# Optimization experiments

Measured on AMD Instinct MI355X. Metric: run time of the kernel, lower is better.

## Reference

```python
import jax, jax.numpy as jnp
import numpy as np

DIM = 1024
LATENT = 512
HEADS = 16
HEAD_DIM = DIM // HEADS


def setup_inputs() -> dict:
    key = jax.random.key(0)
    ks = jax.random.split(key, 9)
    s = 0.02
    return {
        "x": jax.random.normal(ks[0], (2, 2048, DIM), dtype=jnp.float32),
        "Wq": jax.random.normal(ks[1], (DIM, DIM), dtype=jnp.float32) * s,
        "Wkv": jax.random.normal(ks[2], (DIM, 2 * DIM), dtype=jnp.float32) * s,
        "Wk1": jax.random.normal(ks[3], (DIM, LATENT), dtype=jnp.float32) * s,
        "Wk2": jax.random.normal(ks[4], (LATENT, DIM), dtype=jnp.float32) * s,
        "Wv1": jax.random.normal(ks[5], (DIM, LATENT), dtype=jnp.float32) * s,
        "Wv2": jax.random.normal(ks[6], (LATENT, DIM), dtype=jnp.float32) * s,
        "Wo": jax.random.normal(ks[7], (DIM, DIM), dtype=jnp.float32) * s,
        "bo": jax.random.normal(ks[8], (DIM,), dtype=jnp.float32) * s,
    }


def reference(x, Wq, Wkv, Wk1, Wk2, Wv1, Wv2, Wo, bo):
    b, n, dim = x.shape
    scale = HEAD_DIM ** -0.5
    q = x @ Wq                               # [b, n, dim]
    kv = x @ Wkv                             # [b, n, 2*dim]
    k, v = kv[..., :dim], kv[..., dim:]
    # latent bottleneck MLPs (Linear -> ReLU -> Linear, no bias)
    k = jax.nn.relu(k @ Wk1) @ Wk2           # [b, n, dim]
    v = jax.nn.relu(v @ Wv1) @ Wv2           # [b, n, dim]
    # split heads: [b, n, h*d] -> [b, h, n, d]
    def split_heads(t):
        return t.reshape(b, n, HEADS, HEAD_DIM).transpose(0, 2, 1, 3)
    q = split_heads(q) * scale
    k = split_heads(k)
    v = split_heads(v)
    scores = jnp.einsum('bhid,bhjd->bhij', q, k)   # [b, h, n, n]
    attn = jax.nn.softmax(scores, axis=-1)
    out = jnp.einsum('bhij,bhjd->bhid', attn, v)   # [b, h, n, d]
    out = out.transpose(0, 2, 1, 3).reshape(b, n, dim)
    return out @ Wo + bo
```

## Files before the change

### kernel.cpp

```cpp
#include <hip/hip_runtime.h>
#include <stdint.h>


typedef __attribute__((ext_vector_type(8))) __bf16 bf16x8;
typedef __attribute__((ext_vector_type(4))) float f32x4;

__device__ inline unsigned short f2bfu(float f) {
    __bf16 b = (__bf16)f;
    return __builtin_bit_cast(unsigned short, b);
}

__device__ inline float exp2_fast(float f) {
    return __builtin_amdgcn_exp2f(f);
}

__device__ inline void load_lds16(const void* g, void* l) {
    __builtin_amdgcn_global_load_lds(
        (const __attribute__((address_space(1))) uint32_t*)g,
        (__attribute__((address_space(3))) uint32_t*)l, 16, 0, 0);
}

__device__ inline f32x4 mfma_bf16(bf16x8 a, bf16x8 b, f32x4 c) {
    return __builtin_amdgcn_mfma_f32_16x16x32_bf16(a, b, c, 0, 0, 0);
}

__global__ __launch_bounds__(256) void prep_kernel(
    const float* __restrict__ x, unsigned short* __restrict__ xb,
    const float* __restrict__ Wq,  const float* __restrict__ Wo,
    const float* __restrict__ Wkv,
    const float* __restrict__ Wk1, const float* __restrict__ Wv1,
    const float* __restrict__ Wk2, const float* __restrict__ Wv2,
    unsigned short* __restrict__ WqkvT, unsigned short* __restrict__ WoT,
    unsigned short* __restrict__ Wk1T,  unsigned short* __restrict__ Wv1T,
    unsigned short* __restrict__ Wk2T,  unsigned short* __restrict__ Wv2T,
    float qscale)
{
    __shared__ float tile[64][65];
    int id = blockIdx.x;
    int t = threadIdx.x;

    if (id < 4096) {
        int i = (id * 256 + t) * 4;
        float4 v = *(const float4*)&x[i];
        ushort4 o;
        o.x = f2bfu(v.x); o.y = f2bfu(v.y); o.z = f2bfu(v.z); o.w = f2bfu(v.w);
        *(ushort4*)&xb[i] = o;
        return;
    }

    int r = id - 4096;
    const float* src; unsigned short* dst; int R, C; float sc; int bx, by;
    if (r < 512) {
        int z = r >> 8; int rr = r & 255; bx = rr & 15; by = rr >> 4;
        src = z ? Wo : Wq; dst = z ? WoT : WqkvT;
        R = 1024; C = 1024; sc = z ? 1.0f : qscale;
    } else if (r < 1024) {
        int rr = r - 512; bx = rr & 31; by = rr >> 5;
        src = Wkv; dst = WqkvT + 1048576; R = 1024; C = 2048; sc = 1.0f;
    } else if (r < 1280) {
        int rr = r - 1024; int z = rr >> 7; rr &= 127; bx = rr & 7; by = rr >> 3;
        src = z ? Wv1 : Wk1; dst = z ? Wv1T : Wk1T;
        R = 1024; C = 512; sc = 1.0f;
    } else {
        int rr = r - 1280; int z = rr >> 7; rr &= 127; bx = rr & 15; by = rr >> 4;
        src = z ? Wv2 : Wk2; dst = z ? Wv2T : Wk2T;
        R = 512; C = 1024; sc = 1.0f;
    }

    int c0 = bx * 64, r0 = by * 64;
    int col = t & 63, rr4 = t >> 6;
#pragma unroll
    for (int i = 0; i < 16; ++i)
        tile[rr4 + i * 4][col] = src[(size_t)(r0 + rr4 + i * 4) * C + c0 + col];
    __syncthreads();
#pragma unroll
    for (int i = 0; i < 16; ++i) {
        int r2 = rr4 + i * 4;
        dst[(size_t)(c0 + r2) * R + r0 + col] = f2bfu(tile[col][r2] * sc);
    }
}

template<int BN, bool OUTVT = false>
__global__ __launch_bounds__(256) void gemm_bf16_kernel(
    const unsigned short* __restrict__ A0, const unsigned short* __restrict__ A1,
    const unsigned short* __restrict__ B0, const unsigned short* __restrict__ B1,
    void* __restrict__ C0, void* __restrict__ C1,
    int lda, int ldb, int ldc, int K,
    const float* __restrict__ bias, int relu, int out_f32)
{
    const unsigned short* A = blockIdx.z ? A1 : A0;
    const unsigned short* Bt = blockIdx.z ? B1 : B0;
    void* C = blockIdx.z ? C1 : C0;

    constexpr int NI = BN / 32;
    __shared__ unsigned short Als[128 * 32];
    __shared__ unsigned short Bls[BN * 32];
    int t = threadIdx.x;
    int lane = t & 63, w = t >> 6;
    int n0 = blockIdx.x * BN, m0 = blockIdx.y * 128;
    int wm = (w & 1) * 64, wn = (w >> 1) * (BN / 2);
    int lrow = lane & 15, quad = lane >> 4;

    f32x4 acc[4][NI];
    f32x4 z = {0.f, 0.f, 0.f, 0.f};
#pragma unroll
    for (int i = 0; i < 4; ++i)
#pragma unroll
        for (int j = 0; j < NI; ++j) acc[i][j] = z;

    int c0 = t, c1 = t + 256;
    const unsigned short* ag0 = A + (size_t)(m0 + (c0 >> 2)) * lda + (c0 & 3) * 8;
    const unsigned short* ag1 = A + (size_t)(m0 + (c1 >> 2)) * lda + (c1 & 3) * 8;
    const unsigned short* bg0 = Bt + (size_t)(n0 + (c0 >> 2)) * ldb + (c0 & 3) * 8;
    const unsigned short* bg1 = Bt + (size_t)(n0 + ((c1 >> 2) & (BN - 1))) * ldb + (c1 & 3) * 8;

    for (int k0 = 0; k0 < K; k0 += 32) {
        __syncthreads();
        load_lds16(ag0 + k0, &Als[c0 * 8]);
        load_lds16(ag1 + k0, &Als[c1 * 8]);
        load_lds16(bg0 + k0, &Bls[c0 * 8]);
        if constexpr (BN == 128) load_lds16(bg1 + k0, &Bls[c1 * 8]);
        __syncthreads();

        bf16x8 af[4], bfr[NI];
#pragma unroll
        for (int mi = 0; mi < 4; ++mi)
            af[mi] = *(const bf16x8*)&Als[(wm + mi * 16 + lrow) * 32 + quad * 8];
#pragma unroll
        for (int ni = 0; ni < NI; ++ni)
            bfr[ni] = *(const bf16x8*)&Bls[(wn + ni * 16 + lrow) * 32 + quad * 8];
#pragma unroll
        for (int mi = 0; mi < 4; ++mi)
#pragma unroll
            for (int ni = 0; ni < NI; ++ni)
                acc[mi][ni] = mfma_bf16(af[mi], bfr[ni], acc[mi][ni]);
    }

    if (OUTVT && blockIdx.z) {
        int bb = m0 >> 11;
        int npb = (m0 & 2047) + wm;
        unsigned short* vt = (unsigned short*)C;
#pragma unroll
        for (int mi = 0; mi < 4; ++mi)
#pragma unroll
            for (int ni = 0; ni < NI; ++ni) {
                int col = n0 + wn + ni * 16 + lrow;
                int np = npb + mi * 16 + quad * 4;
                ushort4 o;
                o.x = f2bfu(acc[mi][ni][0]);
                o.y = f2bfu(acc[mi][ni][1]);
                o.z = f2bfu(acc[mi][ni][2]);
                o.w = f2bfu(acc[mi][ni][3]);
                *(ushort4*)&vt[(size_t)(bb * 1024 + col) * 2048 + np] = o;
            }
        return;
    }

#pragma unroll
    for (int mi = 0; mi < 4; ++mi)
#pragma unroll
        for (int ni = 0; ni < NI; ++ni)
#pragma unroll
            for (int r = 0; r < 4; ++r) {
                int row = m0 + wm + mi * 16 + quad * 4 + r;
                int col = n0 + wn + ni * 16 + lrow;
                float v = acc[mi][ni][r];
                if (bias) v += bias[col];
                if (relu) v = fmaxf(v, 0.0f);
                if (out_f32) ((float*)C)[(size_t)row * ldc + col] = v;
                else ((unsigned short*)C)[(size_t)row * ldc + col] = f2bfu(v);
            }
}

__global__ __launch_bounds__(256, 2) void flash_mfma_kernel(
    const unsigned short* __restrict__ Q, int ldq,
    const unsigned short* __restrict__ K, int ldk,
    const unsigned short* __restrict__ Vt, unsigned short* __restrict__ O)
{
    __shared__ __align__(16) unsigned short Kls[2][2 * 64 * 32];
    __shared__ __align__(16) unsigned short Vls[2][2 * 64 * 32];
    __shared__ __align__(16) unsigned short Pls[4][2][16 * 64];

    int pbid = blockIdx.x;
    int lbid = (pbid >> 3) + (pbid & 7) * 64;
    int q0 = (lbid & 15) * 128, bh = lbid >> 4;
    int b = bh >> 4, h = bh & 15;
    int t = threadIdx.x;
    int lane = t & 63, w = t >> 6;
    int lrow = lane & 15, quad = lane >> 4;

    bf16x8 qf[2][2];
#pragma unroll
    for (int qb = 0; qb < 2; ++qb) {
        const unsigned short* qrow =
            Q + (size_t)(b * 2048 + q0 + w * 32 + qb * 16 + lrow) * ldq + h * 64;
        qf[qb][0] = *(const bf16x8*)&qrow[quad * 8];
        qf[qb][1] = *(const bf16x8*)&qrow[32 + quad * 8];
    }

    f32x4 z = {0.f, 0.f, 0.f, 0.f};
    f32x4 acco[2][4];
    float m_run[2][4], l_run[2][4];
#pragma unroll
    for (int qb = 0; qb < 2; ++qb)
#pragma unroll
        for (int r = 0; r < 4; ++r) {
            acco[qb][r] = z;
            m_run[qb][r] = -1e30f;
            l_run[qb][r] = 0.f;
        }

    int row4 = t >> 2;
    int seg = (t & 3) * 8;
    const unsigned short* kg = K + (size_t)(b * 2048 + row4) * ldk + h * 64 + seg;
    const unsigned short* vg = Vt + (size_t)(bh * 64 + row4) * 2048 + seg;

    char* pb[2] = { (char*)&Pls[w][0][0], (char*)&Pls[w][1][0] };

    load_lds16(kg,      &Kls[0][t * 8]);
    load_lds16(kg + 32, &Kls[0][2048 + t * 8]);
    load_lds16(vg,      &Vls[0][t * 8]);
    load_lds16(vg + 32, &Vls[0][2048 + t * 8]);
    __syncthreads();

    int cur = 0;
    for (int kt = 0; kt < 2048; kt += 64) {
        if (kt + 64 < 2048) {
            const unsigned short* kgk = kg + (size_t)(kt + 64) * ldk;
            const unsigned short* vgk = vg + kt + 64;
            int nb = cur ^ 1;
            load_lds16(kgk,      &Kls[nb][t * 8]);
            load_lds16(kgk + 32, &Kls[nb][2048 + t * 8]);
            load_lds16(vgk,      &Vls[nb][t * 8]);
            load_lds16(vgk + 32, &Vls[nb][2048 + t * 8]);
        }

        f32x4 s[2][4];
        __builtin_amdgcn_s_setprio(1);
#pragma unroll
        for (int kt8 = 0; kt8 < 4; ++kt8) {
            bf16x8 k0 = *(const bf16x8*)&Kls[cur][(kt8 * 16 + lrow) * 32 + quad * 8];
            bf16x8 k1 = *(const bf16x8*)&Kls[cur][2048 + (kt8 * 16 + lrow) * 32 + quad * 8];
            s[0][kt8] = mfma_bf16(qf[0][0], k0, z);
            s[0][kt8] = mfma_bf16(qf[0][1], k1, s[0][kt8]);
            s[1][kt8] = mfma_bf16(qf[1][0], k0, z);
            s[1][kt8] = mfma_bf16(qf[1][1], k1, s[1][kt8]);
        }
        __builtin_amdgcn_s_setprio(0);

#pragma unroll
        for (int qb = 0; qb < 2; ++qb) {
            float pm[4];
#pragma unroll
            for (int r = 0; r < 4; ++r)
                pm[r] = fmaxf(fmaxf(s[qb][0][r], s[qb][1][r]),
                              fmaxf(s[qb][2][r], s[qb][3][r]));
            bool ok = (pm[0] <= m_run[qb][0] + 8.f) && (pm[1] <= m_run[qb][1] + 8.f)
                   && (pm[2] <= m_run[qb][2] + 8.f) && (pm[3] <= m_run[qb][3] + 8.f);
            if (!__all(ok)) {
#pragma unroll
                for (int r = 0; r < 4; ++r) {
#pragma unroll
                    for (int off = 1; off < 16; off <<= 1)
                        pm[r] = fmaxf(pm[r], __shfl_xor(pm[r], off, 64));
                    float mnew = fmaxf(m_run[qb][r], pm[r]);
                    float al = exp2_fast(m_run[qb][r] - mnew);
                    m_run[qb][r] = mnew;
                    l_run[qb][r] *= al;
#pragma unroll
                    for (int nt = 0; nt < 4; ++nt) acco[qb][nt][r] *= al;
                }
            }
#pragma unroll
            for (int kt8 = 0; kt8 < 4; ++kt8)
#pragma unroll
                for (int r = 0; r < 4; ++r) {
                    float p = exp2_fast(s[qb][kt8][r] - m_run[qb][r]);
                    l_run[qb][r] += p;
                    int row = quad * 4 + r;
                    int boff = (row * 128 + (kt8 * 16 + lrow) * 2) ^ ((row & 7) << 4);
                    *(unsigned short*)(pb[qb] + boff) = f2bfu(p);
                }
        }

        __builtin_amdgcn_s_setprio(1);
#pragma unroll
        for (int ks = 0; ks < 2; ++ks) {
            int rb = (lrow * 128 + ks * 64 + quad * 16) ^ ((lrow & 7) << 4);
            bf16x8 pf0 = *(const bf16x8*)(pb[0] + rb);
            bf16x8 pf1 = *(const bf16x8*)(pb[1] + rb);
#pragma unroll
            for (int nt = 0; nt < 4; ++nt) {
                bf16x8 vf = *(const bf16x8*)&Vls[cur][ks * 2048 + (nt * 16 + lrow) * 32 + quad * 8];
                acco[0][nt] = mfma_bf16(pf0, vf, acco[0][nt]);
                acco[1][nt] = mfma_bf16(pf1, vf, acco[1][nt]);
            }
        }
        __builtin_amdgcn_s_setprio(0);

        __syncthreads();
        cur ^= 1;
    }

#pragma unroll
    for (int qb = 0; qb < 2; ++qb)
#pragma unroll
        for (int r = 0; r < 4; ++r) {
            float lr = l_run[qb][r];
#pragma unroll
            for (int off = 1; off < 16; off <<= 1)
                lr += __shfl_xor(lr, off, 64);
            float rl = 1.0f / lr;
            int row = b * 2048 + q0 + w * 32 + qb * 16 + quad * 4 + r;
#pragma unroll
            for (int nt = 0; nt < 4; ++nt)
                O[(size_t)row * 1024 + h * 64 + nt * 16 + lrow] =
                    f2bfu(acco[qb][nt][r] * rl);
        }
}


extern "C" void kernel_launch(void* const* d_in, const int* in_sizes, int n_in,
                              void* d_out, int out_size, void* d_ws, size_t ws_size,
                              hipStream_t stream) {
    const float* x   = (const float*)d_in[0];
    const float* Wq  = (const float*)d_in[1];
    const float* Wkv = (const float*)d_in[2];
    const float* Wk1 = (const float*)d_in[3];
    const float* Wk2 = (const float*)d_in[4];
    const float* Wv1 = (const float*)d_in[5];
    const float* Wv2 = (const float*)d_in[6];
    const float* Wo  = (const float*)d_in[7];
    const float* bo  = (const float*)d_in[8];
    float* out = (float*)d_out;

    unsigned short* p = (unsigned short*)d_ws;
    unsigned short* xb    = p; p += 4194304;
    unsigned short* WqkvT = p; p += 3145728;
    unsigned short* WoT   = p; p += 1048576;
    unsigned short* Wk1T  = p; p += 524288;
    unsigned short* Wv1T  = p; p += 524288;
    unsigned short* Wk2T  = p; p += 524288;
    unsigned short* Wv2T  = p; p += 524288;
    unsigned short* qkv   = p; p += 12582912;
    unsigned short* tmpb  = p; p += 4194304;
    unsigned short* kvo   = p; p += 8388608;
    unsigned short* vtb   = p; p += 4194304;
    unsigned short* attnb = tmpb;

    dim3 blk(256);
    const float qscale = 0.125f * 1.44269504f;

    prep_kernel<<<5632, blk, 0, stream>>>(
        x, xb, Wq, Wo, Wkv, Wk1, Wv1, Wk2, Wv2,
        WqkvT, WoT, Wk1T, Wv1T, Wk2T, Wv2T, qscale);

    gemm_bf16_kernel<128><<<dim3(24, 32, 1), blk, 0, stream>>>(
        xb, xb, WqkvT, WqkvT, qkv, qkv, 1024, 1024, 3072, 1024, nullptr, 0, 0);
    gemm_bf16_kernel<64><<<dim3(8, 32, 2), blk, 0, stream>>>(
        qkv + 1024, qkv + 2048, Wk1T, Wv1T, tmpb, tmpb + 512,
        3072, 1024, 1024, 1024, nullptr, 1, 0);
    gemm_bf16_kernel<128, true><<<dim3(8, 32, 2), blk, 0, stream>>>(
        tmpb, tmpb + 512, Wk2T, Wv2T, kvo, vtb,
        1024, 512, 1024, 512, nullptr, 0, 0);

    flash_mfma_kernel<<<dim3(512), blk, 0, stream>>>(qkv, 3072, kvo, 1024, vtb, attnb);
    gemm_bf16_kernel<64><<<dim3(16, 32, 1), blk, 0, stream>>>(
        attnb, attnb, WoT, WoT, out, out, 1024, 1024, 1024, 1024, bo, 0, 1);
}
```

Before: 281.3 us.

## Fold Wkv into latent weights to skip the full K/V projection

Precomputes the products of Wk1 and Wv1 with the two halves of Wkv on device, forming a combined Q+latent weight. A single GEMM from x then produces q and the ReLU'd latent k/v together, replacing the separate 2048-wide KV projection and latent GEMM. This cuts GEMM FLOPs and intermediate traffic, but adds a small weight-product GEMM on every call and an extra bf16 rounding of the fused weights.

```diff
diff --git a/kernel.cpp b/kernel.cpp
--- a/kernel.cpp
+++ b/kernel.cpp
@@ -26,8 +26,8 @@
 
 __global__ __launch_bounds__(256) void prep_kernel(
     const float* __restrict__ x, unsigned short* __restrict__ xb,
+    const float* __restrict__ Wkv, unsigned short* __restrict__ Wkvb,
     const float* __restrict__ Wq,  const float* __restrict__ Wo,
-    const float* __restrict__ Wkv,
     const float* __restrict__ Wk1, const float* __restrict__ Wv1,
     const float* __restrict__ Wk2, const float* __restrict__ Wv2,
     unsigned short* __restrict__ WqkvT, unsigned short* __restrict__ WoT,
@@ -39,30 +39,30 @@
     int id = blockIdx.x;
     int t = threadIdx.x;
 
-    if (id < 4096) {
-        int i = (id * 256 + t) * 4;
-        float4 v = *(const float4*)&x[i];
+    if (id < 6144) {
+        const float* s = (id < 4096) ? x : Wkv;
+        unsigned short* d = (id < 4096) ? xb : Wkvb;
+        int base = (id < 4096) ? id : (id - 4096);
+        int i = (base * 256 + t) * 4;
+        float4 v = *(const float4*)&s[i];
         ushort4 o;
         o.x = f2bfu(v.x); o.y = f2bfu(v.y); o.z = f2bfu(v.z); o.w = f2bfu(v.w);
-        *(ushort4*)&xb[i] = o;
+        *(ushort4*)&d[i] = o;
         return;
     }
 
-    int r = id - 4096;
+    int r = id - 6144;
     const float* src; unsigned short* dst; int R, C; float sc; int bx, by;
     if (r < 512) {
         int z = r >> 8; int rr = r & 255; bx = rr & 15; by = rr >> 4;
         src = z ? Wo : Wq; dst = z ? WoT : WqkvT;
         R = 1024; C = 1024; sc = z ? 1.0f : qscale;
-    } else if (r < 1024) {
-        int rr = r - 512; bx = rr & 31; by = rr >> 5;
-        src = Wkv; dst = WqkvT + 1048576; R = 1024; C = 2048; sc = 1.0f;
-    } else if (r < 1280) {
-        int rr = r - 1024; int z = rr >> 7; rr &= 127; bx = rr & 7; by = rr >> 3;
+    } else if (r < 768) {
+        int rr = r - 512; int z = rr >> 7; rr &= 127; bx = rr & 7; by = rr >> 3;
         src = z ? Wv1 : Wk1; dst = z ? Wv1T : Wk1T;
         R = 1024; C = 512; sc = 1.0f;
     } else {
-        int rr = r - 1280; int z = rr >> 7; rr &= 127; bx = rr & 15; by = rr >> 4;
+        int rr = r - 768; int z = rr >> 7; rr &= 127; bx = rr & 15; by = rr >> 4;
         src = z ? Wv2 : Wk2; dst = z ? Wv2T : Wk2T;
         R = 512; C = 1024; sc = 1.0f;
     }
@@ -166,7 +166,7 @@
                 int col = n0 + wn + ni * 16 + lrow;
                 float v = acc[mi][ni][r];
                 if (bias) v += bias[col];
-                if (relu) v = fmaxf(v, 0.0f);
+                if (relu == 1 || (relu == 2 && col >= 1024)) v = fmaxf(v, 0.0f);
                 if (out_f32) ((float*)C)[(size_t)row * ldc + col] = v;
                 else ((unsigned short*)C)[(size_t)row * ldc + col] = f2bfu(v);
             }
@@ -336,35 +336,39 @@
 
     unsigned short* p = (unsigned short*)d_ws;
     unsigned short* xb    = p; p += 4194304;
-    unsigned short* WqkvT = p; p += 3145728;
+    unsigned short* Wkvb  = p; p += 2097152;
+    unsigned short* WqkvT = p; p += 2097152;
     unsigned short* WoT   = p; p += 1048576;
     unsigned short* Wk1T  = p; p += 524288;
     unsigned short* Wv1T  = p; p += 524288;
     unsigned short* Wk2T  = p; p += 524288;
     unsigned short* Wv2T  = p; p += 524288;
-    unsigned short* qkv   = p; p += 12582912;
-    unsigned short* tmpb  = p; p += 4194304;
-    unsigned short* kvo   = p; p += 8388608;
+    unsigned short* qkv2  = p; p += 8388608;
+    unsigned short* attnb = p; p += 4194304;
+    unsigned short* kvo   = p; p += 4194304;
     unsigned short* vtb   = p; p += 4194304;
-    unsigned short* attnb = tmpb;
 
     dim3 blk(256);
     const float qscale = 0.125f * 1.44269504f;
 
-    prep_kernel<<<5632, blk, 0, stream>>>(
-        x, xb, Wq, Wo, Wkv, Wk1, Wv1, Wk2, Wv2,
+    prep_kernel<<<7168, blk, 0, stream>>>(
+        x, xb, Wkv, Wkvb, Wq, Wo, Wk1, Wv1, Wk2, Wv2,
         WqkvT, WoT, Wk1T, Wv1T, Wk2T, Wv2T, qscale);
 
-    gemm_bf16_kernel<128><<<dim3(24, 32, 1), blk, 0, stream>>>(
-        xb, xb, WqkvT, WqkvT, qkv, qkv, 1024, 1024, 3072, 1024, nullptr, 0, 0);
-    gemm_bf16_kernel<64><<<dim3(8, 32, 2), blk, 0, stream>>>(
-        qkv + 1024, qkv + 2048, Wk1T, Wv1T, tmpb, tmpb + 512,
-        3072, 1024, 1024, 1024, nullptr, 1, 0);
+    gemm_bf16_kernel<64><<<dim3(16, 4, 2), blk, 0, stream>>>(
+        Wk1T, Wv1T, Wkvb, Wkvb + 1024,
+        WqkvT + 1024 * 1024, WqkvT + 1536 * 1024,
+        1024, 2048, 1024, 1024, nullptr, 0, 0);
+
+    gemm_bf16_kernel<128><<<dim3(16, 32, 1), blk, 0, stream>>>(
+        xb, xb, WqkvT, WqkvT, qkv2, qkv2, 1024, 1024, 2048, 1024, nullptr, 2, 0);
+
     gemm_bf16_kernel<128, true><<<dim3(8, 32, 2), blk, 0, stream>>>(
-        tmpb, tmpb + 512, Wk2T, Wv2T, kvo, vtb,
-        1024, 512, 1024, 512, nullptr, 0, 0);
-
-    flash_mfma_kernel<<<dim3(512), blk, 0, stream>>>(qkv, 3072, kvo, 1024, vtb, attnb);
+        qkv2 + 1024, qkv2 + 1536, Wk2T, Wv2T, kvo, vtb,
+        2048, 512, 1024, 512, nullptr, 0, 0);
+
+    flash_mfma_kernel<<<dim3(512), blk, 0, stream>>>(qkv2, 2048, kvo, 1024, vtb, attnb);
+
     gemm_bf16_kernel<64><<<dim3(16, 32, 1), blk, 0, stream>>>(
         attnb, attnb, WoT, WoT, out, out, 1024, 1024, 1024, 1024, bo, 0, 1);
 }
```

Result: faster. 262.8 us (-6.6%).
